# Optimization experiments

Hardware: AMD Instinct MI355X
Metric: run time of the kernel (lower is better)

Reference implementation:

```python
import jax, jax.numpy as jnp
import numpy as np

V, E, H, L = 100000, 128, 512, 9
B, T = 64, 512


def setup_inputs() -> dict:
    key = jax.random.key(0)
    ks = jax.random.split(key, 8)
    text = jax.random.randint(ks[0], (B, T), 0, V, dtype=jnp.int32)
    labels = jax.random.randint(ks[1], (B, T), 0, L, dtype=jnp.int32)
    embed = jax.random.normal(ks[2], (V, E), jnp.float32) * 0.02
    Wx = jax.random.normal(ks[3], (E, 4 * H), jnp.float32) * (1.0 / np.sqrt(E))
    Wh = jax.random.normal(ks[4], (H, 4 * H), jnp.float32) * (1.0 / np.sqrt(H))
    # Keras LSTM default: zero bias with unit forget-gate bias (gate order i,f,c,o)
    b = jnp.zeros((4 * H,), jnp.float32).at[H:2 * H].set(1.0)
    Wd = jax.random.normal(ks[5], (H, L), jnp.float32) * (1.0 / np.sqrt(H))
    bd = jnp.zeros((L,), jnp.float32)
    trans = jax.random.uniform(ks[6], (L, L), jnp.float32)
    return dict(text=text, labels=labels, embed=embed, Wx=Wx, Wh=Wh, b=b,
                Wd=Wd, bd=bd, trans=trans)


def _lstm(x, Wx, Wh, b):
    # x: [B,T,E] -> h: [B,T,H]; Keras gate order i,f,c,o
    Bx, Tx, _ = x.shape
    Hh = Wh.shape[0]
    xg = jnp.einsum('bte,eg->btg', x, Wx) + b  # precompute input projections [B,T,4H]

    def step(carry, g_t):
        h, c = carry
        g = g_t + h @ Wh
        i, f, cg, o = jnp.split(g, 4, axis=-1)
        c = jax.nn.sigmoid(f) * c + jax.nn.sigmoid(i) * jnp.tanh(cg)
        h = jax.nn.sigmoid(o) * jnp.tanh(c)
        return (h, c), h

    init = (jnp.zeros((Bx, Hh), x.dtype), jnp.zeros((Bx, Hh), x.dtype))
    _, hs = jax.lax.scan(step, init, jnp.moveaxis(xg, 1, 0))
    return jnp.moveaxis(hs, 0, 1)


def _crf_log_likelihood(logits, labels, lens, trans):
    # tfa.text.crf_log_likelihood: score(seq) - log_norm (forward algorithm)
    Bl, Tl, Ll = logits.shape
    t_idx = jnp.arange(Tl)
    mask = t_idx[None, :] < lens[:, None]  # [B,T]
    unary = jnp.take_along_axis(logits, labels[..., None], axis=2)[..., 0]
    unary = jnp.where(mask, unary, 0.0).sum(-1)
    binary = trans[labels[:, :-1], labels[:, 1:]]
    bmask = t_idx[1:][None, :] < lens[:, None]  # transition t->t+1 counts iff t+1 < len
    binary = jnp.where(bmask, binary, 0.0).sum(-1)
    score = unary + binary

    def step(alpha, xs):
        lg, t = xs  # lg: [B,L]
        new = jax.scipy.special.logsumexp(alpha[:, :, None] + trans[None], axis=1) + lg
        alpha = jnp.where((t < lens)[:, None], new, alpha)
        return alpha, None

    alpha0 = logits[:, 0]
    xs = (jnp.moveaxis(logits[:, 1:], 1, 0), jnp.arange(1, Tl))
    alpha, _ = jax.lax.scan(step, alpha0, xs)
    log_norm = jax.scipy.special.logsumexp(alpha, axis=-1)
    return score - log_norm


def reference(text, labels, embed, Wx, Wh, b, Wd, bd, trans):
    lens = jnp.sum((text != 0).astype(jnp.int32), axis=-1)
    x = embed[text]                      # [B,T,E] (dropout inactive at inference)
    h = _lstm(x, Wx, Wh, b)              # [B,T,H]
    logits = h @ Wd + bd                 # [B,T,L]
    ll = _crf_log_likelihood(logits, labels, lens, trans)  # [B]
    return logits, lens, ll
```

## Files before the change

### kernel.cpp

```cpp
#include <hip/hip_runtime.h>
#include <hip/hip_bf16.h>

#define V_SZ 100000
#define E_SZ 128
#define H_SZ 512
#define L_SZ 9
#define B_SZ 64
#define T_SZ 512
#define G4   (4*H_SZ)

#define LOGITS_N (B_SZ*T_SZ*L_SZ)
#define HS_BYTES ((size_t)B_SZ*T_SZ*H_SZ*2)
#define SENT32 0x7FC07FC0u
#define SENT64 0x7FC07FC07FC07FC0ull

typedef short bf16x8 __attribute__((ext_vector_type(8)));
typedef float f32x4  __attribute__((ext_vector_type(4)));

static __device__ __forceinline__ unsigned short f2bf(float x){
  unsigned int u = __builtin_bit_cast(unsigned int, x);
  unsigned int r = (u + 0x7fffu + ((u >> 16) & 1u)) >> 16;
  return (unsigned short)r;
}
static __device__ __forceinline__ float bf2f(unsigned short b){
  unsigned int u = ((unsigned int)b) << 16;
  return __builtin_bit_cast(float, u);
}
static __device__ __forceinline__ float sig_f(float x){
  return 1.f / (1.f + __expf(-x));
}
static __device__ __forceinline__ float tanh_f(float x){
  float a = fabsf(x);
  float e = __expf(-2.f * a);
  float t = (1.f - e) / (1.f + e);
  return copysignf(t, x);
}

__global__ void k_reset(unsigned long long* __restrict__ hs64){
  const long n = HS_BYTES / 8;
  for (long i = (long)blockIdx.x*256 + threadIdx.x; i < n; i += (long)gridDim.x*256)
    __hip_atomic_store(&hs64[i], SENT64, __ATOMIC_RELAXED, __HIP_MEMORY_SCOPE_AGENT);
}

__global__ void k_lens(const int* __restrict__ text, float* __restrict__ out_lens){
  int b = blockIdx.x;
  int c = 0;
  for (int t = threadIdx.x; t < T_SZ; t += 256)
    c += (text[b*T_SZ + t] != 0);
  for (int off = 32; off; off >>= 1) c += __shfl_down(c, off, 64);
  __shared__ int sred[4];
  int w = threadIdx.x >> 6;
  if ((threadIdx.x & 63) == 0) sred[w] = c;
  __syncthreads();
  if (threadIdx.x == 0)
    out_lens[b] = (float)(sred[0] + sred[1] + sred[2] + sred[3]);
}

__global__ __launch_bounds__(256, 1)
void k_lstm(const int* __restrict__ text, const float* __restrict__ embed,
            const float* __restrict__ Wx, const float* __restrict__ Wh,
            const float* __restrict__ bias, unsigned short* __restrict__ hs)
{
  const int g    = blockIdx.x & 7;
  const int j    = blockIdx.x >> 3;
  const int n0   = j * 16;
  const int tid  = threadIdx.x;
  const int w    = tid >> 6;
  const int lane = tid & 63;
  const int q    = lane >> 4;
  const int l16  = lane & 15;
  const int gate = l16 & 3;
  const int cq   = l16 >> 2;

  __shared__ unsigned short h_lds[2][16*512];
  __shared__ unsigned short x_lds[2][16*128];

  for (int i = tid; i < 2*16*512; i += 256) ((unsigned short*)h_lds)[i] = 0;
  for (int i = tid; i < 2*16*128; i += 256) ((unsigned short*)x_lds)[i] = 0;

  const int hcol = n0 + w*4 + cq;
  const int gcol = gate*H_SZ + hcol;
  bf16x8 Whf[16];
#pragma unroll
  for (int kk = 0; kk < 16; ++kk){
    bf16x8 v;
#pragma unroll
    for (int jj = 0; jj < 8; ++jj)
      v[jj] = (short)f2bf(Wh[(long)(kk*32 + q*8 + jj)*G4 + gcol]);
    Whf[kk] = v;
  }
  bf16x8 Wxf[4];
#pragma unroll
  for (int kk = 0; kk < 4; ++kk){
    bf16x8 v;
#pragma unroll
    for (int jj = 0; jj < 8; ++jj)
      v[jj] = (short)f2bf(Wx[(long)(kk*32 + q*8 + jj)*G4 + gcol]);
    Wxf[kk] = v;
  }
  const float biasv = bias[gcol];

  float cs[4] = {0.f, 0.f, 0.f, 0.f};
  const bool isPub = (gate == 0) && (cq == 0) && (q < 2);

  unsigned short* ppub[4];
#pragma unroll
  for (int rg = 0; rg < 4; ++rg)
    ppub[rg] = hs + ((long)(g*8 + q*4 + rg)*T_SZ)*H_SZ + n0 + w*4;

  const int xr = tid >> 5;
  const int c4 = (tid & 31) * 4;
  const int cb = c4 * 2;
  unsigned short* xdst[2];
#pragma unroll
  for (int pb = 0; pb < 2; ++pb)
    xdst[pb] = (unsigned short*)((char*)x_lds[pb] + xr*256 + (cb ^ (xr << 4)));
  const int* tokp = text + (g*8 + xr)*T_SZ;

  __syncthreads();

  {
    int tok = tokp[0];
    const float4 xv = *(const float4*)(embed + (long)tok*E_SZ + c4);
    unsigned short* pp = xdst[0];
    pp[0] = f2bf(xv.x); pp[1] = f2bf(xv.y); pp[2] = f2bf(xv.z); pp[3] = f2bf(xv.w);
  }

  for (int t = 0; t < T_SZ; ++t){
    const int par = t & 1;

    float4 xv; const bool havex = (t + 1 < T_SZ);
    if (havex){
      int tok = tokp[t + 1];
      xv = *(const float4*)(embed + (long)tok*E_SZ + c4);
    }

    if (t > 0){
      unsigned long long v[4];
      int it = 0; bool ok;
      do {
        ok = true;
#pragma unroll
        for (int c = 0; c < 4; ++c){
          int chunk = tid + 256*c;
          int hr    = chunk >> 7;
          int k4    = chunk & 127;
          v[c] = __hip_atomic_load(
              (const unsigned long long*)(hs + ((long)(g*8 + hr)*T_SZ + (t-1))*H_SZ + k4*4),
              __ATOMIC_RELAXED, __HIP_MEMORY_SCOPE_AGENT);
        }
#pragma unroll
        for (int c = 0; c < 4; ++c){
          unsigned int lo = (unsigned int)v[c], hi = (unsigned int)(v[c] >> 32);
          ok = ok && (lo != SENT32) && (hi != SENT32);
        }
      } while (!ok && ++it < (1 << 20));
#pragma unroll
      for (int c = 0; c < 4; ++c){
        int chunk = tid + 256*c;
        int hr    = chunk >> 7;
        int k4    = chunk & 127;
        *(unsigned long long*)((char*)h_lds[par] + hr*1024 + ((k4*8) ^ (hr << 4))) = v[c];
      }
    }

    asm volatile("s_waitcnt lgkmcnt(0)" ::: "memory");
    __builtin_amdgcn_sched_barrier(0);
    __builtin_amdgcn_s_barrier();
    __builtin_amdgcn_sched_barrier(0);

    f32x4 acc0 = {biasv, biasv, biasv, biasv};
    f32x4 acc1 = {0.f, 0.f, 0.f, 0.f};
#pragma unroll
    for (int kk = 0; kk < 4; ++kk){
      bf16x8 a = *(const bf16x8*)((const char*)x_lds[par] + l16*256 + ((kk*64 + q*16) ^ (l16 << 4)));
      if (kk & 1) acc1 = __builtin_amdgcn_mfma_f32_16x16x32_bf16(a, Wxf[kk], acc1, 0, 0, 0);
      else        acc0 = __builtin_amdgcn_mfma_f32_16x16x32_bf16(a, Wxf[kk], acc0, 0, 0, 0);
    }
    if (t > 0){
#pragma unroll
      for (int kk = 0; kk < 16; ++kk){
        bf16x8 a = *(const bf16x8*)((const char*)h_lds[par] + l16*1024 + ((kk*64 + q*16) ^ (l16 << 4)));
        if (kk & 1) acc1 = __builtin_amdgcn_mfma_f32_16x16x32_bf16(a, Whf[kk], acc1, 0, 0, 0);
        else        acc0 = __builtin_amdgcn_mfma_f32_16x16x32_bf16(a, Whf[kk], acc0, 0, 0, 0);
      }
    }

#pragma unroll
    for (int rg = 0; rg < 4; ++rg){
      float v  = acc0[rg] + acc1[rg];
      float x1 = __shfl_xor(v, 1, 64);
      float x2 = __shfl_xor(v, 2, 64);
      float x3 = __shfl_xor(v, 3, 64);
      float gi = (gate==0)? v : (gate==1)? x1 : (gate==2)? x2 : x3;
      float gf = (gate==1)? v : (gate==0)? x1 : (gate==3)? x2 : x3;
      float gc = (gate==2)? v : (gate==3)? x1 : (gate==0)? x2 : x3;
      float go = (gate==3)? v : (gate==2)? x1 : (gate==1)? x2 : x3;
      cs[rg] = sig_f(gf)*cs[rg] + sig_f(gi)*tanh_f(gc);
      float hv = sig_f(go)*tanh_f(cs[rg]);
      unsigned int hb = (unsigned int)f2bf(hv);
      unsigned int pr  = (unsigned int)__shfl_xor((int)hb, 4, 64);
      unsigned int pk  = hb | (pr << 16);
      unsigned int pk2 = (unsigned int)__shfl_xor((int)pk, 8, 64);
      unsigned long long p8 = (unsigned long long)pk
                            | ((unsigned long long)pk2 << 32);
      if (isPub)
        __hip_atomic_store((unsigned long long*)ppub[rg], p8,
                           __ATOMIC_RELAXED, __HIP_MEMORY_SCOPE_AGENT);
    }
#pragma unroll
    for (int rg = 0; rg < 4; ++rg) ppub[rg] += H_SZ;

    if (havex){
      unsigned short* pp = xdst[par ^ 1];
      pp[0] = f2bf(xv.x); pp[1] = f2bf(xv.y); pp[2] = f2bf(xv.z); pp[3] = f2bf(xv.w);
    }
  }
}

__global__ void k_logits(const unsigned short* __restrict__ hs,
                         const float* __restrict__ Wd, const float* __restrict__ bd,
                         float* __restrict__ out)
{
  __shared__ float wd_s[H_SZ*L_SZ];
  __shared__ float bd_s[L_SZ];
  for (int i = threadIdx.x; i < H_SZ*L_SZ; i += 128) wd_s[i] = Wd[i];
  if (threadIdx.x < L_SZ) bd_s[threadIdx.x] = bd[threadIdx.x];
  __syncthreads();

  long row = (long)blockIdx.x*128 + threadIdx.x;
  const unsigned short* hp = hs + row*H_SZ;
  float acc[9];
#pragma unroll
  for (int jj = 0; jj < 9; ++jj) acc[jj] = 0.f;
  for (int k = 0; k < H_SZ; k += 8){
    uint4 v = *(const uint4*)(hp + k);
    const unsigned short* u = (const unsigned short*)&v;
#pragma unroll
    for (int l = 0; l < 8; ++l){
      float hf = bf2f(u[l]);
#pragma unroll
      for (int jj = 0; jj < 9; ++jj)
        acc[jj] = fmaf(hf, wd_s[(k + l)*L_SZ + jj], acc[jj]);
    }
  }
  float* op = out + row*L_SZ;
#pragma unroll
  for (int jj = 0; jj < 9; ++jj) op[jj] = acc[jj] + bd_s[jj];
}

__global__ void k_crf(const float* __restrict__ logits, const int* __restrict__ labels,
                      const float* __restrict__ trans, const float* __restrict__ lensf,
                      float* __restrict__ out_ll)
{
  int b = blockIdx.x;
  int lane = threadIdx.x;
  int len = (int)lensf[b];
  const float* lg  = logits + (long)b*T_SZ*L_SZ;
  const int*   lab = labels + b*T_SZ;

  float s = 0.f;
  for (int t = lane; t < T_SZ; t += 64){
    if (t < len){
      s += lg[t*L_SZ + lab[t]];
      if (t >= 1) s += trans[lab[t-1]*L_SZ + lab[t]];
    }
  }
  for (int off = 32; off; off >>= 1) s += __shfl_down(s, off, 64);

  float tr[9];
#pragma unroll
  for (int i = 0; i < 9; ++i) tr[i] = (lane < 9) ? trans[i*L_SZ + lane] : 0.f;
  float alpha = (lane < 9) ? lg[lane] : -1e30f;

  for (int t = 1; t < T_SZ; ++t){
    float tmp[9];
#pragma unroll
    for (int i = 0; i < 9; ++i){
      float ai = __shfl(alpha, i, 64);
      tmp[i] = ai + tr[i];
    }
    float m0 = fmaxf(fmaxf(tmp[0], tmp[1]), tmp[2]);
    float m1 = fmaxf(fmaxf(tmp[3], tmp[4]), tmp[5]);
    float m2 = fmaxf(fmaxf(tmp[6], tmp[7]), tmp[8]);
    float m  = fmaxf(fmaxf(m0, m1), m2);
    float e = 0.f;
#pragma unroll
    for (int i = 0; i < 9; ++i) e += __expf(tmp[i] - m);
    float lgv = (lane < 9) ? lg[t*L_SZ + lane] : 0.f;
    float nv = m + __logf(e) + lgv;
    if (t < len && lane < 9) alpha = nv;
  }

  float mm = (lane < 9) ? alpha : -1e30f;
  for (int off = 8; off; off >>= 1) mm = fmaxf(mm, __shfl_down(mm, off, 64));
  mm = __shfl(mm, 0, 64);
  float ee = (lane < 9) ? __expf(alpha - mm) : 0.f;
  for (int off = 8; off; off >>= 1) ee += __shfl_down(ee, off, 64);
  if (lane == 0) out_ll[b] = s - (mm + __logf(ee));
}

extern "C" void kernel_launch(void* const* d_in, const int* in_sizes, int n_in,
                              void* d_out, int out_size, void* d_ws, size_t ws_size,
                              hipStream_t stream)
{
  const int*   text   = (const int*)  d_in[0];
  const int*   labels = (const int*)  d_in[1];
  const float* embed  = (const float*)d_in[2];
  const float* Wx     = (const float*)d_in[3];
  const float* Wh     = (const float*)d_in[4];
  const float* bias   = (const float*)d_in[5];
  const float* Wd     = (const float*)d_in[6];
  const float* bd     = (const float*)d_in[7];
  const float* trans  = (const float*)d_in[8];

  float* out        = (float*)d_out;
  float* out_logits = out;
  float* out_lens   = out + LOGITS_N;
  float* out_ll     = out + LOGITS_N + B_SZ;

  unsigned short* hs = (unsigned short*)d_ws;

  k_reset <<<2048, 256, 0, stream>>>((unsigned long long*)hs);
  k_lens  <<<B_SZ, 256, 0, stream>>>(text, out_lens);
  k_lstm  <<<256, 256, 0, stream>>>(text, embed, Wx, Wh, bias, hs);
  k_logits<<<256, 128, 0, stream>>>(hs, Wd, bd, out_logits);
  k_crf   <<<B_SZ, 64, 0, stream>>>(out_logits, labels, trans, out_lens, out_ll);
}
```

Measured before the change: 1.575 ms.

## Split recurrent h fetch into four phases overlapped with partial MFMA

The recurrent step no longer waits for the whole previous hidden state before computing. It polls and loads h_{t-1} in four column phases, with a block barrier after each phase, and starts the MFMAs on each K-chunk as soon as that chunk is in LDS. This overlaps cross-block spin-waiting and global loads with tensor compute, at the cost of four barriers per timestep instead of one. The sentinel check now looks only at the low 32 bits of each 64-bit word, and the spin limit is raised.

```diff
diff --git a/kernel.cpp b/kernel.cpp
--- a/kernel.cpp
+++ b/kernel.cpp
@@ -108,6 +108,9 @@
   for (int rg = 0; rg < 4; ++rg)
     ppub[rg] = hs + ((long)(g*8 + q*4 + rg)*T_SZ)*H_SZ + n0 + w*4;
 
+  const int hr = tid >> 5;
+  const int c0 = tid & 31;
+
   const int xr = tid >> 5;
   const int c4 = (tid & 31) * 4;
   const int cb = c4 * 2;
@@ -126,6 +129,12 @@
     pp[0] = f2bf(xv.x); pp[1] = f2bf(xv.y); pp[2] = f2bf(xv.z); pp[3] = f2bf(xv.w);
   }
 
+#define RAW_BARRIER() do{ \
+    asm volatile("s_waitcnt lgkmcnt(0)" ::: "memory"); \
+    __builtin_amdgcn_sched_barrier(0); \
+    __builtin_amdgcn_s_barrier(); \
+    __builtin_amdgcn_sched_barrier(0); } while(0)
+
   for (int t = 0; t < T_SZ; ++t){
     const int par = t & 1;
 
@@ -135,54 +144,51 @@
       xv = *(const float4*)(embed + (long)tok*E_SZ + c4);
     }
 
-    if (t > 0){
-      unsigned long long v[4];
-      int it = 0; bool ok;
-      do {
-        ok = true;
-#pragma unroll
-        for (int c = 0; c < 4; ++c){
-          int chunk = tid + 256*c;
-          int hr    = chunk >> 7;
-          int k4    = chunk & 127;
-          v[c] = __hip_atomic_load(
-              (const unsigned long long*)(hs + ((long)(g*8 + hr)*T_SZ + (t-1))*H_SZ + k4*4),
-              __ATOMIC_RELAXED, __HIP_MEMORY_SCOPE_AGENT);
-        }
-#pragma unroll
-        for (int c = 0; c < 4; ++c){
-          unsigned int lo = (unsigned int)v[c], hi = (unsigned int)(v[c] >> 32);
-          ok = ok && (lo != SENT32) && (hi != SENT32);
-        }
-      } while (!ok && ++it < (1 << 20));
-#pragma unroll
-      for (int c = 0; c < 4; ++c){
-        int chunk = tid + 256*c;
-        int hr    = chunk >> 7;
-        int k4    = chunk & 127;
-        *(unsigned long long*)((char*)h_lds[par] + hr*1024 + ((k4*8) ^ (hr << 4))) = v[c];
-      }
-    }
-
-    asm volatile("s_waitcnt lgkmcnt(0)" ::: "memory");
-    __builtin_amdgcn_sched_barrier(0);
-    __builtin_amdgcn_s_barrier();
-    __builtin_amdgcn_sched_barrier(0);
-
     f32x4 acc0 = {biasv, biasv, biasv, biasv};
     f32x4 acc1 = {0.f, 0.f, 0.f, 0.f};
-#pragma unroll
-    for (int kk = 0; kk < 4; ++kk){
-      bf16x8 a = *(const bf16x8*)((const char*)x_lds[par] + l16*256 + ((kk*64 + q*16) ^ (l16 << 4)));
-      if (kk & 1) acc1 = __builtin_amdgcn_mfma_f32_16x16x32_bf16(a, Wxf[kk], acc1, 0, 0, 0);
-      else        acc0 = __builtin_amdgcn_mfma_f32_16x16x32_bf16(a, Wxf[kk], acc0, 0, 0, 0);
-    }
-    if (t > 0){
-#pragma unroll
-      for (int kk = 0; kk < 16; ++kk){
-        bf16x8 a = *(const bf16x8*)((const char*)h_lds[par] + l16*1024 + ((kk*64 + q*16) ^ (l16 << 4)));
-        if (kk & 1) acc1 = __builtin_amdgcn_mfma_f32_16x16x32_bf16(a, Whf[kk], acc1, 0, 0, 0);
-        else        acc0 = __builtin_amdgcn_mfma_f32_16x16x32_bf16(a, Whf[kk], acc0, 0, 0, 0);
+
+    if (t == 0){
+      RAW_BARRIER();
+#pragma unroll
+      for (int kk = 0; kk < 4; ++kk){
+        bf16x8 a = *(const bf16x8*)((const char*)x_lds[par] + l16*256 + ((kk*64 + q*16) ^ (l16 << 4)));
+        if (kk & 1) acc1 = __builtin_amdgcn_mfma_f32_16x16x32_bf16(a, Wxf[kk], acc1, 0, 0, 0);
+        else        acc0 = __builtin_amdgcn_mfma_f32_16x16x32_bf16(a, Wxf[kk], acc0, 0, 0, 0);
+      }
+    } else {
+      const unsigned long long* hp8 = (const unsigned long long*)hs
+          + ((long)(g*8 + hr)*T_SZ + (t-1))*(H_SZ/4) + c0;
+      unsigned long long v = __hip_atomic_load(hp8, __ATOMIC_RELAXED,
+                                               __HIP_MEMORY_SCOPE_AGENT);
+#pragma unroll
+      for (int ph = 0; ph < 4; ++ph){
+        int it = 0;
+        while ((unsigned int)v == SENT32 && ++it < (1 << 22))
+          v = __hip_atomic_load(hp8 + ph*32, __ATOMIC_RELAXED,
+                                __HIP_MEMORY_SCOPE_AGENT);
+        {
+          int k4 = ph*32 + c0;
+          *(unsigned long long*)((char*)h_lds[par] + hr*1024 + ((k4*8) ^ (hr << 4))) = v;
+        }
+        if (ph < 3)
+          v = __hip_atomic_load(hp8 + (ph+1)*32, __ATOMIC_RELAXED,
+                                __HIP_MEMORY_SCOPE_AGENT);
+        RAW_BARRIER();
+        if (ph == 0){
+#pragma unroll
+          for (int kk = 0; kk < 4; ++kk){
+            bf16x8 a = *(const bf16x8*)((const char*)x_lds[par] + l16*256 + ((kk*64 + q*16) ^ (l16 << 4)));
+            if (kk & 1) acc1 = __builtin_amdgcn_mfma_f32_16x16x32_bf16(a, Wxf[kk], acc1, 0, 0, 0);
+            else        acc0 = __builtin_amdgcn_mfma_f32_16x16x32_bf16(a, Wxf[kk], acc0, 0, 0, 0);
+          }
+        }
+#pragma unroll
+        for (int kz = 0; kz < 4; ++kz){
+          int kk = ph*4 + kz;
+          bf16x8 a = *(const bf16x8*)((const char*)h_lds[par] + l16*1024 + ((kk*64 + q*16) ^ (l16 << 4)));
+          if (kk & 1) acc1 = __builtin_amdgcn_mfma_f32_16x16x32_bf16(a, Whf[kk], acc1, 0, 0, 0);
+          else        acc0 = __builtin_amdgcn_mfma_f32_16x16x32_bf16(a, Whf[kk], acc0, 0, 0, 0);
+        }
       }
     }
 
@@ -216,6 +222,7 @@
       pp[0] = f2bf(xv.x); pp[1] = f2bf(xv.y); pp[2] = f2bf(xv.z); pp[3] = f2bf(xv.w);
     }
   }
+#undef RAW_BARRIER
 }
 
 __global__ void k_logits(const unsigned short* __restrict__ hs,
```

Result: slower. 1.893 ms (+20.2%).

## Halve LSTM block count with 512-thread blocks covering 32 hidden columns

Applied to the files above, without the earlier changes.

The persistent LSTM kernel now launches 128 blocks of 512 threads instead of 256 blocks of 256, so each block owns 32 hidden columns across 8 waves. This halves the number of blocks that must exchange h through global memory each timestep, while each block does twice the MFMA work. The spin-wait on published h now reloads only the chunks still holding the sentinel, with each thread polling 2 chunks, and it checks only the low word. Embedding loads shrink to float2 per thread. The risk is a longer per-step critical path inside each block in exchange for cheaper cross-block synchronisation.

```diff
diff --git a/kernel.cpp b/kernel.cpp
--- a/kernel.cpp
+++ b/kernel.cpp
@@ -56,14 +56,14 @@
     out_lens[b] = (float)(sred[0] + sred[1] + sred[2] + sred[3]);
 }
 
-__global__ __launch_bounds__(256, 1)
+__global__ __launch_bounds__(512, 1)
 void k_lstm(const int* __restrict__ text, const float* __restrict__ embed,
             const float* __restrict__ Wx, const float* __restrict__ Wh,
             const float* __restrict__ bias, unsigned short* __restrict__ hs)
 {
   const int g    = blockIdx.x & 7;
   const int j    = blockIdx.x >> 3;
-  const int n0   = j * 16;
+  const int n0   = j * 32;
   const int tid  = threadIdx.x;
   const int w    = tid >> 6;
   const int lane = tid & 63;
@@ -75,8 +75,8 @@
   __shared__ unsigned short h_lds[2][16*512];
   __shared__ unsigned short x_lds[2][16*128];
 
-  for (int i = tid; i < 2*16*512; i += 256) ((unsigned short*)h_lds)[i] = 0;
-  for (int i = tid; i < 2*16*128; i += 256) ((unsigned short*)x_lds)[i] = 0;
+  for (int i = tid; i < 2*16*512; i += 512) ((unsigned short*)h_lds)[i] = 0;
+  for (int i = tid; i < 2*16*128; i += 512) ((unsigned short*)x_lds)[i] = 0;
 
   const int hcol = n0 + w*4 + cq;
   const int gcol = gate*H_SZ + hcol;
@@ -108,9 +108,14 @@
   for (int rg = 0; rg < 4; ++rg)
     ppub[rg] = hs + ((long)(g*8 + q*4 + rg)*T_SZ)*H_SZ + n0 + w*4;
 
-  const int xr = tid >> 5;
-  const int c4 = (tid & 31) * 4;
-  const int cb = c4 * 2;
+  const int hr0 = tid >> 7;
+  const int k40 = tid & 127;
+  const int hr1 = hr0 + 4;
+  const int k41 = k40;
+
+  const int xr = tid >> 6;
+  const int c2 = (tid & 63) * 2;
+  const int cb = c2 * 2;
   unsigned short* xdst[2];
 #pragma unroll
   for (int pb = 0; pb < 2; ++pb)
@@ -121,47 +126,39 @@
 
   {
     int tok = tokp[0];
-    const float4 xv = *(const float4*)(embed + (long)tok*E_SZ + c4);
+    const float2 xv = *(const float2*)(embed + (long)tok*E_SZ + c2);
     unsigned short* pp = xdst[0];
-    pp[0] = f2bf(xv.x); pp[1] = f2bf(xv.y); pp[2] = f2bf(xv.z); pp[3] = f2bf(xv.w);
+    pp[0] = f2bf(xv.x); pp[1] = f2bf(xv.y);
   }
 
   for (int t = 0; t < T_SZ; ++t){
     const int par = t & 1;
 
-    float4 xv; const bool havex = (t + 1 < T_SZ);
+    float2 xv; const bool havex = (t + 1 < T_SZ);
     if (havex){
       int tok = tokp[t + 1];
-      xv = *(const float4*)(embed + (long)tok*E_SZ + c4);
+      xv = *(const float2*)(embed + (long)tok*E_SZ + c2);
     }
 
     if (t > 0){
-      unsigned long long v[4];
-      int it = 0; bool ok;
-      do {
-        ok = true;
-#pragma unroll
-        for (int c = 0; c < 4; ++c){
-          int chunk = tid + 256*c;
-          int hr    = chunk >> 7;
-          int k4    = chunk & 127;
-          v[c] = __hip_atomic_load(
-              (const unsigned long long*)(hs + ((long)(g*8 + hr)*T_SZ + (t-1))*H_SZ + k4*4),
-              __ATOMIC_RELAXED, __HIP_MEMORY_SCOPE_AGENT);
-        }
-#pragma unroll
-        for (int c = 0; c < 4; ++c){
-          unsigned int lo = (unsigned int)v[c], hi = (unsigned int)(v[c] >> 32);
-          ok = ok && (lo != SENT32) && (hi != SENT32);
-        }
-      } while (!ok && ++it < (1 << 20));
-#pragma unroll
-      for (int c = 0; c < 4; ++c){
-        int chunk = tid + 256*c;
-        int hr    = chunk >> 7;
-        int k4    = chunk & 127;
-        *(unsigned long long*)((char*)h_lds[par] + hr*1024 + ((k4*8) ^ (hr << 4))) = v[c];
+      const unsigned long long* p0 = (const unsigned long long*)
+          (hs + ((long)(g*8 + hr0)*T_SZ + (t-1))*H_SZ + k40*4);
+      const unsigned long long* p1 = (const unsigned long long*)
+          (hs + ((long)(g*8 + hr1)*T_SZ + (t-1))*H_SZ + k41*4);
+      unsigned long long v0 = __hip_atomic_load(p0, __ATOMIC_RELAXED,
+                                                __HIP_MEMORY_SCOPE_AGENT);
+      unsigned long long v1 = __hip_atomic_load(p1, __ATOMIC_RELAXED,
+                                                __HIP_MEMORY_SCOPE_AGENT);
+      int it = 0;
+      while ((((unsigned int)v0 == SENT32) | ((unsigned int)v1 == SENT32))
+             && ++it < (1 << 21)){
+        if ((unsigned int)v0 == SENT32)
+          v0 = __hip_atomic_load(p0, __ATOMIC_RELAXED, __HIP_MEMORY_SCOPE_AGENT);
+        if ((unsigned int)v1 == SENT32)
+          v1 = __hip_atomic_load(p1, __ATOMIC_RELAXED, __HIP_MEMORY_SCOPE_AGENT);
       }
+      *(unsigned long long*)((char*)h_lds[par] + hr0*1024 + ((k40*8) ^ (hr0 << 4))) = v0;
+      *(unsigned long long*)((char*)h_lds[par] + hr1*1024 + ((k41*8) ^ (hr1 << 4))) = v1;
     }
 
     asm volatile("s_waitcnt lgkmcnt(0)" ::: "memory");
@@ -213,7 +210,7 @@
 
     if (havex){
       unsigned short* pp = xdst[par ^ 1];
-      pp[0] = f2bf(xv.x); pp[1] = f2bf(xv.y); pp[2] = f2bf(xv.z); pp[3] = f2bf(xv.w);
+      pp[0] = f2bf(xv.x); pp[1] = f2bf(xv.y);
     }
   }
 }
@@ -323,7 +320,7 @@
 
   k_reset <<<2048, 256, 0, stream>>>((unsigned long long*)hs);
   k_lens  <<<B_SZ, 256, 0, stream>>>(text, out_lens);
-  k_lstm  <<<256, 256, 0, stream>>>(text, embed, Wx, Wh, bias, hs);
+  k_lstm  <<<128, 512, 0, stream>>>(text, embed, Wx, Wh, bias, hs);
   k_logits<<<256, 128, 0, stream>>>(hs, Wd, bd, out_logits);
   k_crf   <<<B_SZ, 64, 0, stream>>>(out_logits, labels, trans, out_lens, out_ll);
 }
```

Measured after the change: 1.817 ms. +15.4%, slower.
